# Optimization experiments

Measured on AMD Instinct MI355X. Metric: run time of the kernel, lower is better.

The kernel has to match this reference:

```python
import jax, jax.numpy as jnp
import numpy as np

N_POINTS = 2_000_000
IN_CH = 10
OUT_CH = 32  # out_channel // 2 for non-last layer
NUM_PILLARS = 100_000
BN_EPS = 1e-3


def setup_inputs() -> dict:
    key = jax.random.key(0)
    k1, k2, k3, k4 = jax.random.split(key, 4)
    inputs = jax.random.normal(k1, (N_POINTS, IN_CH), dtype=jnp.float32)
    unq_inv = jax.random.randint(k2, (N_POINTS,), 0, NUM_PILLARS, dtype=jnp.int32)
    # Linear params (PyTorch nn.Linear: y = x @ W.T + b)
    W = jax.random.normal(k3, (OUT_CH, IN_CH), dtype=jnp.float32) * (1.0 / np.sqrt(IN_CH))
    b = jax.random.normal(k4, (OUT_CH,), dtype=jnp.float32) * 0.01
    # BatchNorm1d affine params
    gamma = jnp.ones((OUT_CH,), dtype=jnp.float32)
    beta = jnp.zeros((OUT_CH,), dtype=jnp.float32)
    return {"inputs": inputs, "W": W, "b": b, "gamma": gamma, "beta": beta,
            "unq_inv": unq_inv, "num_pillars": NUM_PILLARS}


def reference(inputs, W, b, gamma, beta, unq_inv, num_pillars):
    # Linear: [N, in] -> [N, out]
    v = inputs @ W.T + b
    # BatchNorm1d (training-mode batch stats, biased variance, eps=1e-3)
    mean = jnp.mean(v, axis=0)
    var = jnp.mean(jnp.square(v - mean), axis=0)
    xn = (v - mean) * jax.lax.rsqrt(var + BN_EPS) * gamma + beta
    x = jax.nn.relu(xn)
    # scatter_max over pillars (segment max along dim 0)
    x_max = jax.ops.segment_max(x, unq_inv, num_segments=num_pillars)  # [P, out]
    # gather back per point and average with per-point features
    return (x + x_max[unq_inv]) * 0.5
```

## Files before the change

### kernel.cpp

```cpp
#include <hip/hip_runtime.h>
#include <hip/hip_fp16.h>

#define NPTS    2000000
#define PIL     100000
#define BN_EPS_F 1e-3f

#define SHIFT   5
#define PPB     32
#define NBKT    3125
#define NBAC    256
#define CHUNK   7813
#define TILE    128

#define ACC_OFF    0
#define WPH_OFF    512
#define BP_OFF     768
#define PART_OFF   1024
#define TOTS_OFF   17920
#define STARTS_OFF 21248
#define HIST_OFF   24576
#define PSA_OFF    839680
#define PSB_OFF    8839680

__device__ __forceinline__ constexpr int tri_idx(int j, int k) {
    return j * 10 - j * (j - 1) / 2 + (k - j);
}

__device__ __forceinline__ unsigned pk2(float x, float y) {
    __half2 h = __floats2half2_rn(x, y);
    return *reinterpret_cast<unsigned*>(&h);
}
__device__ __forceinline__ float2 uph2(unsigned u) {
    __half2 h = *reinterpret_cast<__half2*>(&u);
    return __half22float2(h);
}

__global__ __launch_bounds__(512) void kA_hist(const int* __restrict__ unq,
                                               unsigned* __restrict__ hist)
{
    __shared__ unsigned h[NBKT];
    for (int i = threadIdx.x; i < NBKT; i += 512) h[i] = 0u;
    __syncthreads();
    const int lo = blockIdx.x * CHUNK;
    const int hi = min(lo + CHUNK, NPTS);
    for (int t = lo + threadIdx.x; t < hi; t += 512)
        atomicAdd(&h[unq[t] >> SHIFT], 1u);
    __syncthreads();
    for (int i = threadIdx.x; i < NBKT; i += 512)
        hist[(size_t)blockIdx.x * NBKT + i] = h[i];
}

__global__ __launch_bounds__(64) void kB1_colsum(const unsigned* __restrict__ hist,
                                                 unsigned* __restrict__ tots)
{
    const int c = blockIdx.x, lane = threadIdx.x;
    unsigned s = 0;
#pragma unroll
    for (int i = 0; i < NBAC / 64; ++i) s += hist[(size_t)(i * 64 + lane) * NBKT + c];
#pragma unroll
    for (int sh = 1; sh < 64; sh <<= 1) s += __shfl_xor(s, sh, 64);
    if (lane == 0) tots[c] = s;
}

__global__ __launch_bounds__(1024) void kB2_scan(const unsigned* __restrict__ tots,
                                                 unsigned* __restrict__ starts)
{
    __shared__ unsigned ps[1024];
    const int t = threadIdx.x;
    unsigned v[4], sum = 0;
#pragma unroll
    for (int i = 0; i < 4; ++i) {
        int idx = t * 4 + i;
        v[i] = (idx < NBKT) ? tots[idx] : 0u;
        sum += v[i];
    }
    ps[t] = sum;
    __syncthreads();
    for (int d = 1; d < 1024; d <<= 1) {
        unsigned x = (t >= d) ? ps[t - d] : 0u;
        __syncthreads();
        ps[t] += x;
        __syncthreads();
    }
    unsigned excl = ps[t] - sum;
#pragma unroll
    for (int i = 0; i < 4; ++i) {
        int idx = t * 4 + i;
        if (idx < NBKT) starts[idx] = excl;
        excl += v[i];
    }
    if (t == 1023) starts[NBKT] = ps[1023];
}

__global__ __launch_bounds__(64) void kB3_expand(unsigned* __restrict__ hist,
                                                 const unsigned* __restrict__ starts)
{
    const int c = blockIdx.x, lane = threadIdx.x;
    unsigned hv[NBAC / 64];
    unsigned psum = 0;
#pragma unroll
    for (int i = 0; i < NBAC / 64; ++i) {
        hv[i] = hist[(size_t)(lane * (NBAC / 64) + i) * NBKT + c];
        psum += hv[i];
    }
    unsigned incl = psum;
#pragma unroll
    for (int s = 1; s < 64; s <<= 1) {
        unsigned v = __shfl_up(incl, s, 64);
        if (lane >= s) incl += v;
    }
    unsigned run = starts[c] + (incl - psum);
#pragma unroll
    for (int i = 0; i < NBAC / 64; ++i) {
        hist[(size_t)(lane * (NBAC / 64) + i) * NBKT + c] = run;
        run += hv[i];
    }
}

__global__ __launch_bounds__(512) void kC2_scatter_mom(const float* __restrict__ in,
                                                       const int* __restrict__ unq,
                                                       const unsigned* __restrict__ off,
                                                       uint4* __restrict__ psA4,
                                                       uint2* __restrict__ psB2,
                                                       float* __restrict__ partial)
{
    __shared__ unsigned cur[NBKT];
    __shared__ float lds2[8][66];
    for (int i = threadIdx.x; i < NBKT; i += 512)
        cur[i] = off[(size_t)blockIdx.x * NBKT + i];
    __syncthreads();

    float acc[65];
#pragma unroll
    for (int i = 0; i < 65; ++i) acc[i] = 0.f;

    const int lo = blockIdx.x * CHUNK;
    const int hi = min(lo + CHUNK, NPTS);
    for (int t = lo + threadIdx.x; t < hi; t += 512) {
        int pil = unq[t];
        unsigned slot = atomicAdd(&cur[pil >> SHIFT], 1u);
        const float* px = in + (size_t)t * 10;
        float4 r0 = *reinterpret_cast<const float4*>(px);
        float4 r1 = *reinterpret_cast<const float4*>(px + 4);
        float2 r2 = *reinterpret_cast<const float2*>(px + 8);
        unsigned meta = ((unsigned)(pil & (PPB - 1)) << 21) | (unsigned)t;
        psA4[slot] = make_uint4(pk2(r0.x, r0.y), pk2(r0.z, r0.w),
                                pk2(r1.x, r1.y), pk2(r1.z, r1.w));
        psB2[slot] = make_uint2(pk2(r2.x, r2.y), meta);

        float xf[10] = { r0.x, r0.y, r0.z, r0.w, r1.x, r1.y, r1.z, r1.w, r2.x, r2.y };
#pragma unroll
        for (int j = 0; j < 10; ++j) acc[j] += xf[j];
        int o = 10;
#pragma unroll
        for (int j = 0; j < 10; ++j)
#pragma unroll
            for (int k = j; k < 10; ++k) acc[o++] += xf[j] * xf[k];
    }

#pragma unroll
    for (int i = 0; i < 65; ++i) {
        float v = acc[i];
#pragma unroll
        for (int s = 1; s < 64; s <<= 1) v += __shfl_xor(v, s, 64);
        acc[i] = v;
    }
    const int wid = threadIdx.x >> 6, lane = threadIdx.x & 63;
    if (lane == 0) {
#pragma unroll
        for (int i = 0; i < 65; ++i) lds2[wid][i] = acc[i];
    }
    __syncthreads();
    if (threadIdx.x < 65) {
        float s = 0.f;
#pragma unroll
        for (int wv = 0; wv < 8; ++wv) s += lds2[wv][threadIdx.x];
        partial[(size_t)threadIdx.x * NBAC + blockIdx.x] = s;
    }
}

__global__ void k1_final(const float* __restrict__ partial, float* __restrict__ accum)
{
    const int e = blockIdx.x, lane = threadIdx.x;
    float s = 0.f;
#pragma unroll
    for (int i = 0; i < NBAC / 64; ++i) s += partial[(size_t)e * NBAC + i * 64 + lane];
#pragma unroll
    for (int sh = 1; sh < 64; sh <<= 1) s += __shfl_xor(s, sh, 64);
    if (lane == 0) accum[e] = s;
}

__global__ void k2_finalize(const float* __restrict__ accum, const float* __restrict__ W,
                            const float* __restrict__ b, const float* __restrict__ gamma,
                            const float* __restrict__ beta, unsigned* __restrict__ Wph,
                            float* __restrict__ bp)
{
    int c = threadIdx.x;
    if (c >= 32) return;
    const float invN = 1.0f / (float)NPTS;
    float m[10], w[10];
#pragma unroll
    for (int k = 0; k < 10; ++k) m[k] = accum[k] * invN;
#pragma unroll
    for (int k = 0; k < 10; ++k) w[k] = W[c*10 + k];
    float mean = b[c];
#pragma unroll
    for (int k = 0; k < 10; ++k) mean += w[k] * m[k];
    float var = 0.f;
#pragma unroll
    for (int j = 0; j < 10; ++j) {
#pragma unroll
        for (int k = j; k < 10; ++k) {
            float Cjk = accum[10 + tri_idx(j, k)] * invN - m[j] * m[k];
            var += w[j] * w[k] * Cjk * ((j == k) ? 1.f : 2.f);
        }
    }
    float scale = gamma[c] * rsqrtf(var + BN_EPS_F);
#pragma unroll
    for (int j = 0; j < 5; ++j)
        Wph[c*5 + j] = pk2(w[2*j] * scale, w[2*j + 1] * scale);
    bp[c] = (b[c] - mean) * scale + beta[c];
}

#define STAGE_LOAD(ci_next, ra, rb)                                           \
    {                                                                         \
        size_t aB = (size_t)(s0 + (unsigned)(ci_next) * TILE) * 4;            \
        size_t bB = (size_t)(s0 + (unsigned)(ci_next) * TILE) * 2;            \
        if (aB + TILE * 4 <= gendA) {                                         \
            ra = *reinterpret_cast<const uint2*>(psA + aB + threadIdx.x * 2); \
            rb = psB[bB + threadIdx.x];                                       \
        } else {                                                              \
            size_t i0 = aB + threadIdx.x * 2;                                 \
            ra.x = psA[i0 < gendA ? i0 : gendA - 1];                          \
            ra.y = psA[i0 + 1 < gendA ? i0 + 1 : gendA - 1];                  \
            size_t i1 = bB + threadIdx.x;                                     \
            rb = psB[i1 < gendB ? i1 : gendB - 1];                            \
        }                                                                     \
    }
#define STAGE_WRITE(buf, ra, rb)                                              \
    {                                                                         \
        ldsA[buf][threadIdx.x * 2]     = ra.x;                                \
        ldsA[buf][threadIdx.x * 2 + 1] = ra.y;                                \
        ldsB[buf][threadIdx.x]         = rb;                                  \
    }

__global__ __launch_bounds__(256) void kD10_reduce(const unsigned* __restrict__ psA,
                                                   const unsigned* __restrict__ psB,
                                                   const unsigned* __restrict__ starts,
                                                   const unsigned* __restrict__ Wph,
                                                   const float* __restrict__ bp,
                                                   float* __restrict__ out)
{
    __shared__ unsigned tab[PPB * 32];
    __shared__ unsigned ldsA[2][TILE * 4];
    __shared__ unsigned ldsB[2][TILE * 2];
    for (int i = threadIdx.x; i < PPB * 32; i += 256) tab[i] = 0u;

    const int c   = threadIdx.x & 31;
    const int sub = threadIdx.x >> 5;
    float2 w[5];
#pragma unroll
    for (int j = 0; j < 5; ++j) w[j] = uph2(Wph[c * 5 + j]);
    const float bc = bp[c];

    const unsigned s0 = starts[blockIdx.x];
    const unsigned s1 = starts[blockIdx.x + 1];
    const unsigned nrec = s1 - s0;
    const int nch = (int)((nrec + TILE - 1) / TILE);
    const size_t gendA = (size_t)NPTS * 4;
    const size_t gendB = (size_t)NPTS * 2;

    uint2 ra; unsigned rb;
    if (nch > 0) { STAGE_LOAD(0, ra, rb); STAGE_WRITE(0, ra, rb); }
    __syncthreads();
    for (int ci = 0; ci < nch; ++ci) {
        const bool more = (ci + 1 < nch);
        if (more) STAGE_LOAD(ci + 1, ra, rb);
        const unsigned* lA = ldsA[ci & 1];
        const unsigned* lB = ldsB[ci & 1];
        int rem = (int)nrec - ci * TILE;
        int rmax = rem < TILE ? rem : TILE;
        for (int r = sub; r < rmax; r += 8) {
            uint4 A = *reinterpret_cast<const uint4*>(lA + r * 4);
            uint2 B = *reinterpret_cast<const uint2*>(lB + r * 2);
            float2 x0 = uph2(A.x), x1 = uph2(A.y), x2 = uph2(A.z),
                   x3 = uph2(A.w), x4 = uph2(B.x);
            unsigned pl = (B.y >> 21) & (PPB - 1);
            float a = fmaf(x0.x, w[0].x, bc);
            a = fmaf(x0.y, w[0].y, a);
            a = fmaf(x1.x, w[1].x, a); a = fmaf(x1.y, w[1].y, a);
            a = fmaf(x2.x, w[2].x, a); a = fmaf(x2.y, w[2].y, a);
            a = fmaf(x3.x, w[3].x, a); a = fmaf(x3.y, w[3].y, a);
            a = fmaf(x4.x, w[4].x, a); a = fmaf(x4.y, w[4].y, a);
            a = fmaxf(a, 0.f);
            atomicMax(&tab[(pl << 5) + c], __float_as_uint(a));
        }
        __syncthreads();
        if (more) STAGE_WRITE((ci + 1) & 1, ra, rb);
        __syncthreads();
    }

    if (nch > 0) { STAGE_LOAD(0, ra, rb); STAGE_WRITE(0, ra, rb); }
    __syncthreads();
    for (int ci = 0; ci < nch; ++ci) {
        const bool more = (ci + 1 < nch);
        if (more) STAGE_LOAD(ci + 1, ra, rb);
        const unsigned* lA = ldsA[ci & 1];
        const unsigned* lB = ldsB[ci & 1];
        int rem = (int)nrec - ci * TILE;
        int rmax = rem < TILE ? rem : TILE;
        for (int r = sub; r < rmax; r += 8) {
            uint4 A = *reinterpret_cast<const uint4*>(lA + r * 4);
            uint2 B = *reinterpret_cast<const uint2*>(lB + r * 2);
            float2 x0 = uph2(A.x), x1 = uph2(A.y), x2 = uph2(A.z),
                   x3 = uph2(A.w), x4 = uph2(B.x);
            unsigned idx = B.y & 0x1FFFFFu;
            unsigned pl = (B.y >> 21) & (PPB - 1);
            float a = fmaf(x0.x, w[0].x, bc);
            a = fmaf(x0.y, w[0].y, a);
            a = fmaf(x1.x, w[1].x, a); a = fmaf(x1.y, w[1].y, a);
            a = fmaf(x2.x, w[2].x, a); a = fmaf(x2.y, w[2].y, a);
            a = fmaf(x3.x, w[3].x, a); a = fmaf(x3.y, w[3].y, a);
            a = fmaf(x4.x, w[4].x, a); a = fmaf(x4.y, w[4].y, a);
            a = fmaxf(a, 0.f);
            float mx = __uint_as_float(tab[(pl << 5) + c]);
            __builtin_nontemporal_store((a + mx) * 0.5f, &out[(size_t)idx * 32 + c]);
        }
        __syncthreads();
        if (more) STAGE_WRITE((ci + 1) & 1, ra, rb);
        __syncthreads();
    }
}

extern "C" void kernel_launch(void* const* d_in, const int* in_sizes, int n_in,
                              void* d_out, int out_size, void* d_ws, size_t ws_size,
                              hipStream_t stream)
{
    const float* in    = (const float*)d_in[0];
    const float* W     = (const float*)d_in[1];
    const float* b     = (const float*)d_in[2];
    const float* gamma = (const float*)d_in[3];
    const float* beta  = (const float*)d_in[4];
    const int*   unq   = (const int*)d_in[5];

    float* ws      = (float*)d_ws;
    float* accum   = ws + ACC_OFF;
    unsigned* Wph  = (unsigned*)(ws + WPH_OFF);
    float* bp      = ws + BP_OFF;
    float* partial = ws + PART_OFF;
    unsigned* tots   = (unsigned*)(ws + TOTS_OFF);
    unsigned* starts = (unsigned*)(ws + STARTS_OFF);
    unsigned* hist   = (unsigned*)(ws + HIST_OFF);
    unsigned* psA    = (unsigned*)(ws + PSA_OFF);
    unsigned* psB    = (unsigned*)(ws + PSB_OFF);

    kA_hist<<<NBAC, 512, 0, stream>>>(unq, hist);
    kB1_colsum<<<NBKT, 64, 0, stream>>>(hist, tots);
    kB2_scan<<<1, 1024, 0, stream>>>(tots, starts);
    kB3_expand<<<NBKT, 64, 0, stream>>>(hist, starts);
    kC2_scatter_mom<<<NBAC, 512, 0, stream>>>(in, unq, hist,
                                              (uint4*)psA, (uint2*)psB, partial);
    k1_final<<<65, 64, 0, stream>>>(partial, accum);
    k2_finalize<<<1, 64, 0, stream>>>(accum, W, b, gamma, beta, Wph, bp);
    kD10_reduce<<<NBKT, 256, 0, stream>>>(psA, psB, starts, Wph, bp, (float*)d_out);
}
```

Measured before the change: 177.5 us.

## Fuse moment finalize kernels, double bucketing blocks, widen reduce tile staging

Merges the two tiny BN-statistics finalize kernels into one 1024-thread block, removing a launch and the global round trip through accum. Doubles the number of histogram/scatter blocks (NBAC 256→512, smaller CHUNK) with workspace offsets adjusted. Doubles the reduce kernel's staging tile to 256 records, loading with uint4/uint2 vector loads and vector LDS writes, so there are fewer chunk iterations and barriers per bucket. The larger histogram array raises the work in the column-sum pass, and the bigger tile uses more LDS.

```diff
diff --git a/kernel.cpp b/kernel.cpp
--- a/kernel.cpp
+++ b/kernel.cpp
@@ -8,19 +8,18 @@
 #define SHIFT   5
 #define PPB     32
 #define NBKT    3125
-#define NBAC    256
-#define CHUNK   7813
-#define TILE    128
-
-#define ACC_OFF    0
+#define NBAC    512
+#define CHUNK   3907
+#define TILE    256
+
 #define WPH_OFF    512
 #define BP_OFF     768
 #define PART_OFF   1024
-#define TOTS_OFF   17920
-#define STARTS_OFF 21248
-#define HIST_OFF   24576
-#define PSA_OFF    839680
-#define PSB_OFF    8839680
+#define TOTS_OFF   34816
+#define STARTS_OFF 38400
+#define HIST_OFF   49152
+#define PSA_OFF    1654784
+#define PSB_OFF    9654784
 
 __device__ __forceinline__ constexpr int tri_idx(int j, int k) {
     return j * 10 - j * (j - 1) / 2 + (k - j);
@@ -179,72 +178,80 @@
     }
 }
 
-__global__ void k1_final(const float* __restrict__ partial, float* __restrict__ accum)
-{
-    const int e = blockIdx.x, lane = threadIdx.x;
-    float s = 0.f;
-#pragma unroll
-    for (int i = 0; i < NBAC / 64; ++i) s += partial[(size_t)e * NBAC + i * 64 + lane];
-#pragma unroll
-    for (int sh = 1; sh < 64; sh <<= 1) s += __shfl_xor(s, sh, 64);
-    if (lane == 0) accum[e] = s;
-}
-
-__global__ void k2_finalize(const float* __restrict__ accum, const float* __restrict__ W,
-                            const float* __restrict__ b, const float* __restrict__ gamma,
-                            const float* __restrict__ beta, unsigned* __restrict__ Wph,
-                            float* __restrict__ bp)
-{
-    int c = threadIdx.x;
-    if (c >= 32) return;
-    const float invN = 1.0f / (float)NPTS;
-    float m[10], w[10];
-#pragma unroll
-    for (int k = 0; k < 10; ++k) m[k] = accum[k] * invN;
-#pragma unroll
-    for (int k = 0; k < 10; ++k) w[k] = W[c*10 + k];
-    float mean = b[c];
-#pragma unroll
-    for (int k = 0; k < 10; ++k) mean += w[k] * m[k];
-    float var = 0.f;
-#pragma unroll
-    for (int j = 0; j < 10; ++j) {
-#pragma unroll
-        for (int k = j; k < 10; ++k) {
-            float Cjk = accum[10 + tri_idx(j, k)] * invN - m[j] * m[k];
-            var += w[j] * w[k] * Cjk * ((j == k) ? 1.f : 2.f);
+__global__ __launch_bounds__(1024) void k12_final(const float* __restrict__ partial,
+                                                  const float* __restrict__ W,
+                                                  const float* __restrict__ b,
+                                                  const float* __restrict__ gamma,
+                                                  const float* __restrict__ beta,
+                                                  unsigned* __restrict__ Wph,
+                                                  float* __restrict__ bp)
+{
+    __shared__ float acc_s[65];
+    const int t = threadIdx.x;
+    if (t < 65 * 8) {
+        const int e = t >> 3, j = t & 7;
+        float s = 0.f;
+        const float* p = partial + (size_t)e * NBAC + j * 64;
+#pragma unroll
+        for (int i = 0; i < 64; ++i) s += p[i];
+#pragma unroll
+        for (int sh = 1; sh < 8; sh <<= 1) s += __shfl_xor(s, sh, 64);
+        if (j == 0) acc_s[e] = s;
+    }
+    __syncthreads();
+    if (t < 32) {
+        const int c = t;
+        const float invN = 1.0f / (float)NPTS;
+        float m[10], w[10];
+#pragma unroll
+        for (int k = 0; k < 10; ++k) m[k] = acc_s[k] * invN;
+#pragma unroll
+        for (int k = 0; k < 10; ++k) w[k] = W[c*10 + k];
+        float mean = b[c];
+#pragma unroll
+        for (int k = 0; k < 10; ++k) mean += w[k] * m[k];
+        float var = 0.f;
+#pragma unroll
+        for (int j = 0; j < 10; ++j) {
+#pragma unroll
+            for (int k = j; k < 10; ++k) {
+                float Cjk = acc_s[10 + tri_idx(j, k)] * invN - m[j] * m[k];
+                var += w[j] * w[k] * Cjk * ((j == k) ? 1.f : 2.f);
+            }
         }
-    }
-    float scale = gamma[c] * rsqrtf(var + BN_EPS_F);
-#pragma unroll
-    for (int j = 0; j < 5; ++j)
-        Wph[c*5 + j] = pk2(w[2*j] * scale, w[2*j + 1] * scale);
-    bp[c] = (b[c] - mean) * scale + beta[c];
-}
-
-#define STAGE_LOAD(ci_next, ra, rb)                                           \
-    {                                                                         \
-        size_t aB = (size_t)(s0 + (unsigned)(ci_next) * TILE) * 4;            \
-        size_t bB = (size_t)(s0 + (unsigned)(ci_next) * TILE) * 2;            \
-        if (aB + TILE * 4 <= gendA) {                                         \
-            ra = *reinterpret_cast<const uint2*>(psA + aB + threadIdx.x * 2); \
-            rb = psB[bB + threadIdx.x];                                       \
-        } else {                                                              \
-            size_t i0 = aB + threadIdx.x * 2;                                 \
-            ra.x = psA[i0 < gendA ? i0 : gendA - 1];                          \
-            ra.y = psA[i0 + 1 < gendA ? i0 + 1 : gendA - 1];                  \
-            size_t i1 = bB + threadIdx.x;                                     \
-            rb = psB[i1 < gendB ? i1 : gendB - 1];                            \
-        }                                                                     \
-    }
-#define STAGE_WRITE(buf, ra, rb)                                              \
-    {                                                                         \
-        ldsA[buf][threadIdx.x * 2]     = ra.x;                                \
-        ldsA[buf][threadIdx.x * 2 + 1] = ra.y;                                \
-        ldsB[buf][threadIdx.x]         = rb;                                  \
-    }
-
-__global__ __launch_bounds__(256) void kD10_reduce(const unsigned* __restrict__ psA,
+        float scale = gamma[c] * rsqrtf(var + BN_EPS_F);
+#pragma unroll
+        for (int j = 0; j < 5; ++j)
+            Wph[c*5 + j] = pk2(w[2*j] * scale, w[2*j + 1] * scale);
+        bp[c] = (b[c] - mean) * scale + beta[c];
+    }
+}
+
+#define STAGE_LOAD(ci_next, ra, rb)                                              \
+    {                                                                            \
+        size_t aB = (size_t)(s0 + (unsigned)(ci_next) * TILE) * 4;               \
+        size_t bB = (size_t)(s0 + (unsigned)(ci_next) * TILE) * 2;               \
+        if (aB + TILE * 4 <= gendA) {                                            \
+            ra = *reinterpret_cast<const uint4*>(psA + aB + threadIdx.x * 4);    \
+            rb = *reinterpret_cast<const uint2*>(psB + bB + threadIdx.x * 2);    \
+        } else {                                                                 \
+            size_t i0 = aB + threadIdx.x * 4;                                    \
+            ra.x = psA[i0     < gendA ? i0     : gendA - 1];                     \
+            ra.y = psA[i0 + 1 < gendA ? i0 + 1 : gendA - 1];                     \
+            ra.z = psA[i0 + 2 < gendA ? i0 + 2 : gendA - 1];                     \
+            ra.w = psA[i0 + 3 < gendA ? i0 + 3 : gendA - 1];                     \
+            size_t i1 = bB + threadIdx.x * 2;                                    \
+            rb.x = psB[i1     < gendB ? i1     : gendB - 1];                     \
+            rb.y = psB[i1 + 1 < gendB ? i1 + 1 : gendB - 1];                     \
+        }                                                                        \
+    }
+#define STAGE_WRITE(buf, ra, rb)                                                 \
+    {                                                                            \
+        *reinterpret_cast<uint4*>(&ldsA[buf][threadIdx.x * 4]) = ra;             \
+        *reinterpret_cast<uint2*>(&ldsB[buf][threadIdx.x * 2]) = rb;             \
+    }
+
+__global__ __launch_bounds__(256) void kD11_reduce(const unsigned* __restrict__ psA,
                                                    const unsigned* __restrict__ psB,
                                                    const unsigned* __restrict__ starts,
                                                    const unsigned* __restrict__ Wph,
@@ -270,7 +277,7 @@
     const size_t gendA = (size_t)NPTS * 4;
     const size_t gendB = (size_t)NPTS * 2;
 
-    uint2 ra; unsigned rb;
+    uint4 ra; uint2 rb;
     if (nch > 0) { STAGE_LOAD(0, ra, rb); STAGE_WRITE(0, ra, rb); }
     __syncthreads();
     for (int ci = 0; ci < nch; ++ci) {
@@ -344,7 +351,6 @@
     const int*   unq   = (const int*)d_in[5];
 
     float* ws      = (float*)d_ws;
-    float* accum   = ws + ACC_OFF;
     unsigned* Wph  = (unsigned*)(ws + WPH_OFF);
     float* bp      = ws + BP_OFF;
     float* partial = ws + PART_OFF;
@@ -360,7 +366,6 @@
     kB3_expand<<<NBKT, 64, 0, stream>>>(hist, starts);
     kC2_scatter_mom<<<NBAC, 512, 0, stream>>>(in, unq, hist,
                                               (uint4*)psA, (uint2*)psB, partial);
-    k1_final<<<65, 64, 0, stream>>>(partial, accum);
-    k2_finalize<<<1, 64, 0, stream>>>(accum, W, b, gamma, beta, Wph, bp);
-    kD10_reduce<<<NBKT, 256, 0, stream>>>(psA, psB, starts, Wph, bp, (float*)d_out);
-}
+    k12_final<<<1, 1024, 0, stream>>>(partial, W, b, gamma, beta, Wph, bp);
+    kD11_reduce<<<NBKT, 256, 0, stream>>>(psA, psB, starts, Wph, bp, (float*)d_out);
+}
```

After: 206.2 us. 1.16x slower.
